# Performance work log

Hardware: AMD Instinct MI355X
Metric: run time of the kernel (lower is better)

Reference implementation:

```python
import jax, jax.numpy as jnp
import numpy as np

CUTOFF = 5.0
N_GAUSS = 32
N_HEADS = 8
MAX_Z = 100


def _gather(feat, idx):
    # feat: (B, N, ...), idx: (B, N, K) -> (B, N, K, ...)
    return jax.vmap(lambda f, i: f[i])(feat, idx)


def setup_inputs() -> dict:
    key = jax.random.key(0)
    ks = jax.random.split(key, 10)
    B, N, K, D, G = 16, 512, 48, 128, N_GAUSS
    s = 0.05
    positions = jax.random.normal(ks[0], (B, N, 3), dtype=jnp.float32) * 2.0
    z = jax.random.randint(ks[1], (B, N), 0, MAX_Z)
    neighbors = jax.random.randint(ks[2], (B, N, K), 0, N)
    neighbor_mask = jnp.ones((B, N, K), dtype=jnp.float32)
    embedding = jax.random.normal(ks[3], (MAX_Z, D), jnp.float32)
    embedding = embedding.at[0].set(0.0)  # padding_idx=0
    filt_W = jax.random.normal(ks[4], (G, D), jnp.float32) * s
    filt_b = jnp.zeros((D,), jnp.float32)
    Wq = jax.random.normal(ks[5], (D, D), jnp.float32) * s
    Wk = jax.random.normal(ks[6], (D, D), jnp.float32) * s
    Wv = jax.random.normal(ks[7], (D, D), jnp.float32) * s
    Wo = jax.random.normal(ks[8], (D, D), jnp.float32) * s
    return dict(positions=positions, z=z, neighbors=neighbors,
                neighbor_mask=neighbor_mask, embedding=embedding,
                filt_W=filt_W, filt_b=filt_b, Wq=Wq, Wk=Wk, Wv=Wv, Wo=Wo)


def reference(positions, z, neighbors, neighbor_mask, embedding,
              filt_W, filt_b, Wq, Wk, Wv, Wo):
    B, N, K = neighbors.shape
    D = embedding.shape[1]
    H = N_HEADS
    hd = D // H

    # atom embeddings
    x = embedding[z]                                        # (B, N, D)

    # AtomDistances: neighbor gather + distances
    pos_j = _gather(positions, neighbors)                   # (B, N, K, 3)
    r_vec = pos_j - positions[:, :, None, :]
    r_ij = jnp.sqrt(jnp.sum(r_vec * r_vec, axis=-1) + 1e-12)  # (B, N, K)

    # Positional_Embedding: prepend self-distance 0.01, log-normal smearing
    r_iij = jnp.concatenate(
        [jnp.full((B, N, 1), 0.01, r_ij.dtype), r_ij], axis=-1)  # (B, N, K+1)
    offsets = jnp.linspace(np.log(0.1), np.log(CUTOFF), N_GAUSS).astype(r_ij.dtype)
    width = offsets[1] - offsets[0]
    coeff = -0.5 / (width * width)
    f_iij = jnp.exp(coeff * (jnp.log(r_iij)[..., None] - offsets) ** 2)  # (B,N,K+1,G)

    # filter network + cosine cutoff
    W = f_iij @ filt_W + filt_b                             # (B, N, K+1, D)
    C = 0.5 * (jnp.cos(r_iij * jnp.pi / CUTOFF) + 1.0) * (r_iij < CUTOFF)
    W = W * C[..., None]

    # gather neighbor embeddings, include self (ego) node
    x_j = _gather(x, neighbors)                             # (B, N, K, D)
    nodes = jnp.concatenate([x[:, :, None, :], x_j], axis=2)  # (B, N, K+1, D)
    kv_in = nodes * W

    # EgoAttention: center atom attends over {self + neighbors}
    q = (x @ Wq).reshape(B, N, H, hd)
    k = (kv_in @ Wk).reshape(B, N, K + 1, H, hd)
    v = (kv_in @ Wv).reshape(B, N, K + 1, H, hd)
    scores = jnp.einsum('bnhd,bnkhd->bnhk', q, k) / jnp.sqrt(jnp.float32(hd))
    mask = jnp.concatenate(
        [jnp.ones((B, N, 1), neighbor_mask.dtype), neighbor_mask], axis=-1)
    scores = jnp.where(mask[:, :, None, :] > 0, scores, jnp.float32(-1e9))
    attn = jax.nn.softmax(scores, axis=-1)
    agg = jnp.einsum('bnhk,bnkhd->bnhd', attn, v).reshape(B, N, D)
    v_msg = agg @ Wo

    # residual update (apply_transition_function=False): x = x + v
    return x + v_msg
```

## Files before the change

### kernel.cpp

```cpp
#include <hip/hip_runtime.h>
#include <math.h>

#define NTHREADS 256

typedef _Float16 v8h __attribute__((ext_vector_type(8)));
typedef float    v4f __attribute__((ext_vector_type(4)));

namespace {
constexpr int D   = 128;
constexpr int H   = 8;
constexpr int KNB = 48;
constexpr int KP1 = 49;
constexpr int NN  = 512;

constexpr size_t WS_P    = 0;
constexpr size_t WS_QKZ  = 16777216;
constexpr size_t WS_WVOT = 16982016;
constexpr size_t WS_QZ   = 17244160;
constexpr size_t WS_FWTP = 17295360;
constexpr size_t WS_EMBH = 17303552;
constexpr size_t WS_NEED = 17329152;

constexpr float LOG_LO = -2.302585092994046f;
constexpr float LOG_HI =  1.609437912434100f;
constexpr float GWIDTH = (LOG_HI - LOG_LO) / 31.0f;
constexpr float GCOEFF = -0.5f / (GWIDTH * GWIDTH);
constexpr float PI_OVER_CUT = 3.14159265358979323846f / 5.0f;
}

union H8U4 { _Float16 h[8]; uint4 u; };
union H4U2 { _Float16 h[4]; uint2 u; };

__global__ __launch_bounds__(NTHREADS) void k0a_qz(
    const float* __restrict__ embedding, const float* __restrict__ Wq,
    float* __restrict__ qz) {
  const int idx = blockIdx.x * NTHREADS + threadIdx.x;
  const int zz = idx >> 7, j = idx & 127;
  float a0 = 0.f, a1 = 0.f, a2 = 0.f, a3 = 0.f;
  for (int e = 0; e < 128; e += 4) {
    a0 = fmaf(embedding[zz * 128 + e + 0], Wq[(e + 0) * 128 + j], a0);
    a1 = fmaf(embedding[zz * 128 + e + 1], Wq[(e + 1) * 128 + j], a1);
    a2 = fmaf(embedding[zz * 128 + e + 2], Wq[(e + 2) * 128 + j], a2);
    a3 = fmaf(embedding[zz * 128 + e + 3], Wq[(e + 3) * 128 + j], a3);
  }
  qz[idx] = (a0 + a1) + (a2 + a3);
}

__global__ __launch_bounds__(NTHREADS) void k0b_prep(
    const float* __restrict__ filt_W, const float* __restrict__ Wk,
    const float* __restrict__ Wv, const float* __restrict__ Wo,
    const float* __restrict__ qz, const float* __restrict__ embedding,
    _Float16* __restrict__ QKz, _Float16* __restrict__ WvoT,
    _Float16* __restrict__ fWTP, _Float16* __restrict__ embh) {
  const int blk = blockIdx.x;
  const int tid = threadIdx.x;
  if (blk < 400) {
    const int idx = blk * NTHREADS + tid;
    const int zz = idx >> 10, hc = idx & 1023, h = hc >> 7, c = hc & 127;
    float acc = 0.0f;
#pragma unroll
    for (int e = 0; e < 16; ++e)
      acc = fmaf(qz[zz * 128 + h * 16 + e], Wk[c * 128 + h * 16 + e], acc);
    QKz[idx] = (_Float16)(acc * 0.25f);
  } else if (blk < 912) {
    const int idx = (blk - 400) * NTHREADS + tid;
    const int cp = idx >> 10, kk = idx & 1023, d = kk >> 3, h = kk & 7;
    float acc = 0.0f;
#pragma unroll
    for (int cc = 0; cc < 16; ++cc)
      acc = fmaf(Wv[d * 128 + h * 16 + cc], Wo[(h * 16 + cc) * 128 + cp], acc);
    WvoT[idx] = (_Float16)acc;
  } else if (blk < 914) {
    const int i = (blk - 912) * NTHREADS + tid;
    const int nt = i >> 6, quad = (i >> 4) & 3, col = i & 15;
    H8U4 pk;
#pragma unroll
    for (int j = 0; j < 8; ++j)
      pk.h[j] = (_Float16)filt_W[(quad * 8 + j) * 128 + nt * 16 + col];
    *(uint4*)&fWTP[i * 8] = pk.u;
  } else {
    const int idx = (blk - 914) * NTHREADS + tid;
    embh[idx] = (_Float16)embedding[idx];
  }
}

namespace k2c {
constexpr int KV_S  = 136;
constexpr int QK_S  = 136;
constexpr int ATH_S = 72;
constexpr int SC_S  = 52;
constexpr int OFF_KV  = 0;
constexpr int OFF_QK  = 13328;
constexpr int OFF_ATH = 15504;
constexpr int OFF_SC  = 16800;
constexpr int OFF_LR  = 18464;
constexpr int OFF_C   = 18672;
constexpr int OFF_MSK = 18880;
constexpr int OFF_ZJ  = 19088;
constexpr int SMEM    = 19296;
}

__global__ __launch_bounds__(NTHREADS, 8) void k2_attn(
    const float* __restrict__ positions, const int* __restrict__ z,
    const int* __restrict__ neighbors, const float* __restrict__ nmask,
    const _Float16* __restrict__ embh, const float* __restrict__ filt_b,
    const _Float16* __restrict__ fWTP, const _Float16* __restrict__ QKz,
    _Float16* __restrict__ P) {
  using namespace k2c;
  __shared__ __align__(16) char smem[SMEM];
  _Float16* s_kv  = reinterpret_cast<_Float16*>(smem + OFF_KV);
  _Float16* s_qk  = reinterpret_cast<_Float16*>(smem + OFF_QK);
  _Float16* s_ath = reinterpret_cast<_Float16*>(smem + OFF_ATH);
  float*    s_sc  = reinterpret_cast<float*>(smem + OFF_SC);
  float*    s_lr  = reinterpret_cast<float*>(smem + OFF_LR);
  float*    s_C   = reinterpret_cast<float*>(smem + OFF_C);
  float*    s_msk = reinterpret_cast<float*>(smem + OFF_MSK);
  int*      s_zj  = reinterpret_cast<int*>(smem + OFF_ZJ);

  const int a   = blockIdx.x;
  const int b   = a >> 9;
  const int n   = a & (NN - 1);
  const int tid = threadIdx.x;
  const int w    = tid >> 6;
  const int lane = tid & 63;
  const int col  = lane & 15;
  const int quad = lane >> 4;

  const int zc = __builtin_amdgcn_readfirstlane(z[a]);

  if (tid < KP1) {
    int j; float m;
    if (tid == 0) { j = n; m = 1.0f; }
    else { j = neighbors[a * KNB + tid - 1]; m = nmask[a * KNB + tid - 1]; }
    float r;
    if (tid == 0) r = 0.01f;
    else {
      const float dx = positions[(b * NN + j) * 3 + 0] - positions[a * 3 + 0];
      const float dy = positions[(b * NN + j) * 3 + 1] - positions[a * 3 + 1];
      const float dz = positions[(b * NN + j) * 3 + 2] - positions[a * 3 + 2];
      r = sqrtf(dx * dx + dy * dy + dz * dz + 1e-12f);
    }
    s_lr[tid]  = __logf(r);
    s_C[tid]   = (r < 5.0f) ? (0.5f * (__cosf(r * PI_OVER_CUT) + 1.0f)) : 0.0f;
    s_msk[tid] = m;
    s_zj[tid]  = z[b * NN + j];
  } else if (tid >= 128) {
    const int i = tid - 128;
    const uint4 v = *(const uint4*)(QKz + (size_t)zc * 1024 + i * 8);
    const int h = i >> 4, dd = (i & 15) * 8;
    *(uint4*)&s_qk[h * QK_S + dd] = v;
  }
  __syncthreads();

  {
    const int trow = 16 * w + col;
    const float lr = s_lr[trow < KP1 ? trow : KP1 - 1];
    v8h afrag;
#pragma unroll
    for (int j = 0; j < 8; ++j) {
      const int g = quad * 8 + j;
      const float dlt = lr - (LOG_LO + (float)g * GWIDTH);
      afrag[j] = (_Float16)__expf(GCOEFF * dlt * dlt);
    }
    v4f acc[8];
#pragma unroll
    for (int nt = 0; nt < 8; ++nt) {
      const v8h bfrag = *(const v8h*)(fWTP + (((nt * 4 + quad) * 16 + col) * 8));
      v4f zero = {0.0f, 0.0f, 0.0f, 0.0f};
      acc[nt] = __builtin_amdgcn_mfma_f32_16x16x32_f16(afrag, bfrag, zero, 0, 0, 0);
    }
    float bv[8];
#pragma unroll
    for (int nt = 0; nt < 8; ++nt) bv[nt] = filt_b[nt * 16 + col];
#pragma unroll
    for (int reg = 0; reg < 4; ++reg) {
      const int t = 16 * w + quad * 4 + reg;
      const bool valid = t < KP1;
      const float cf = valid ? s_C[t] : 0.0f;
      const int   zj = s_zj[valid ? t : KP1 - 1];
      const _Float16* erow = embh + (size_t)zj * D;
#pragma unroll
      for (int nt = 0; nt < 8; ++nt) {
        const int c = nt * 16 + col;
        if (valid)
          s_kv[t * KV_S + c] =
              (_Float16)((acc[nt][reg] + bv[nt]) * cf * (float)erow[c]);
      }
    }
  }
  __syncthreads();

  {
    v4f sacc = {0.0f, 0.0f, 0.0f, 0.0f};
#pragma unroll
    for (int ks = 0; ks < 4; ++ks) {
      const v8h afr = *(const v8h*)&s_kv[(16 * w + col) * KV_S + ks * 32 + quad * 8];
      const v8h bfr = *(const v8h*)&s_qk[col * QK_S + ks * 32 + quad * 8];
      sacc = __builtin_amdgcn_mfma_f32_16x16x32_f16(afr, bfr, sacc, 0, 0, 0);
    }
    const int h = col;
    if (h < H) {
#pragma unroll
      for (int reg = 0; reg < 4; ++reg) {
        const int t = 16 * w + quad * 4 + reg;
        if (t < KP1) {
          float sc = sacc[reg];
          if (s_msk[t] <= 0.0f) sc = -1e9f;
          s_sc[h * SC_S + t] = sc;
        }
      }
    }
  }
  __syncthreads();

  if (tid < 64) {
    const int h  = tid >> 3;
    const int sl = tid & 7;
    float* row = &s_sc[h * SC_S];
    float m = -1e30f;
    for (int t = sl; t < KP1; t += 8) m = fmaxf(m, row[t]);
    m = fmaxf(m, __shfl_xor(m, 1));
    m = fmaxf(m, __shfl_xor(m, 2));
    m = fmaxf(m, __shfl_xor(m, 4));
    float s = 0.0f;
    float ev[7];
#pragma unroll
    for (int i = 0; i < 7; ++i) {
      const int t = sl + i * 8;
      const float e = (t < KP1) ? __expf(row[t] - m) : 0.0f;
      ev[i] = e;
      s += e;
    }
    s += __shfl_xor(s, 1);
    s += __shfl_xor(s, 2);
    s += __shfl_xor(s, 4);
    const float inv = 1.0f / s;
#pragma unroll
    for (int i = 0; i < 7; ++i) {
      const int t = sl + i * 8;
      if (t < KP1) s_ath[h * ATH_S + t] = (_Float16)(ev[i] * inv);
    }
  } else if (tid < 128) {
    const int i = tid - 64;
    for (int idx = i; idx < 8 * 15; idx += 64) {
      const int h = idx / 15;
      const int t = KP1 + idx % 15;
      s_ath[h * ATH_S + t] = (_Float16)0.0f;
    }
  }
  __syncthreads();

  {
    const int arow = (col < 8) ? col : 8;
    const v8h a0 = *(const v8h*)&s_ath[arow * ATH_S + quad * 8];
    const v8h a1 = *(const v8h*)&s_ath[arow * ATH_S + 32 + quad * 8];
#pragma unroll
    for (int nti = 0; nti < 2; ++nti) {
      const int c = (2 * w + nti) * 16 + col;
      v8h b0, b1;
#pragma unroll
      for (int j = 0; j < 8; ++j) {
        b0[j] = s_kv[(quad * 8 + j) * KV_S + c];
        const int t1 = 32 + quad * 8 + j;
        const _Float16 vv = s_kv[t1 * KV_S + c];
        b1[j] = (t1 < KP1) ? vv : (_Float16)0.0f;
      }
      v4f pacc = {0.0f, 0.0f, 0.0f, 0.0f};
      pacc = __builtin_amdgcn_mfma_f32_16x16x32_f16(a0, b0, pacc, 0, 0, 0);
      pacc = __builtin_amdgcn_mfma_f32_16x16x32_f16(a1, b1, pacc, 0, 0, 0);
      if (quad < 2) {
        H4U2 pk;
#pragma unroll
        for (int reg = 0; reg < 4; ++reg) pk.h[reg] = (_Float16)pacc[reg];
        *(uint2*)(P + (size_t)a * 1024 + c * 8 + quad * 4) = pk.u;
      }
    }
  }
}

__global__ __launch_bounds__(NTHREADS) void k3_gemm(
    const int* __restrict__ z, const float* __restrict__ embedding,
    const _Float16* __restrict__ P, const _Float16* __restrict__ WvoT,
    float* __restrict__ out) {
  __shared__ __align__(16) _Float16 sA[16 * 136];
  __shared__ __align__(16) _Float16 sB[64 * 136];
  __shared__ int s_z[16];
  const int a0 = (blockIdx.x >> 1) * 16;
  const int n0 = (blockIdx.x & 1) * 64;
  const int tid = threadIdx.x;
  const int w    = tid >> 6;
  const int lane = tid & 63;
  const int col  = lane & 15;
  const int quad = lane >> 4;
  if (tid < 16) s_z[tid] = z[a0 + tid];

  v4f acc = (v4f){0.f, 0.f, 0.f, 0.f};

  for (int kc = 0; kc < 8; ++kc) {
    const int k0 = kc * 128;
    __syncthreads();
    {
      const int ai = tid >> 4, sl = tid & 15;
      *(uint4*)&sA[ai * 136 + sl * 8] =
          *(const uint4*)(P + (size_t)(a0 + ai) * 1024 + k0 + sl * 8);
    }
#pragma unroll
    for (int it = 0; it < 4; ++it) {
      const int idx = it * NTHREADS + tid;
      const int cp = idx >> 4, sl = idx & 15;
      *(uint4*)&sB[cp * 136 + sl * 8] =
          *(const uint4*)(WvoT + (size_t)(n0 + cp) * 1024 + k0 + sl * 8);
    }
    __syncthreads();
#pragma unroll
    for (int ks = 0; ks < 4; ++ks) {
      const v8h af = *(const v8h*)&sA[col * 136 + ks * 32 + quad * 8];
      const v8h bf = *(const v8h*)&sB[(w * 16 + col) * 136 + ks * 32 + quad * 8];
      acc = __builtin_amdgcn_mfma_f32_16x16x32_f16(af, bf, acc, 0, 0, 0);
    }
  }
#pragma unroll
  for (int reg = 0; reg < 4; ++reg) {
    const int al = quad * 4 + reg;
    const int cp = n0 + w * 16 + col;
    out[(size_t)(a0 + al) * 128 + cp] =
        embedding[(size_t)s_z[al] * 128 + cp] + acc[reg];
  }
}

namespace mono {
constexpr int KV_S = 136, QK_S = 136, FWT_S = 40, ATH_S = 64, SC_S = 52, P_S = 132;
constexpr int OFF_KV = 0, OFF_FWT = 17408, OFF_P = 17408, OFF_AGG = 21632,
              OFF_QK = 27648, OFF_ATH = 32000, OFF_SC = 34048, OFF_Q = 35712,
              OFF_LR = 36224, OFF_C = 36432, OFF_MSK = 36640, OFF_ZJ = 36848,
              SMEM = 37056;
}

__global__ __launch_bounds__(NTHREADS, 4) void tdt_mono(
    const float* __restrict__ positions, const int* __restrict__ z,
    const int* __restrict__ neighbors, const float* __restrict__ nmask,
    const float* __restrict__ embedding, const float* __restrict__ filt_W,
    const float* __restrict__ filt_b, const float* __restrict__ Wq,
    const float* __restrict__ Wk, const float* __restrict__ Wv,
    const float* __restrict__ Wo, float* __restrict__ out) {
  using namespace mono;
  __shared__ __align__(16) char smem[SMEM];
  _Float16* s_kvh = reinterpret_cast<_Float16*>(smem + OFF_KV);
  _Float16* s_fWT = reinterpret_cast<_Float16*>(smem + OFF_FWT);
  float*    s_p   = reinterpret_cast<float*>(smem + OFF_P);
  float*    s_agg = reinterpret_cast<float*>(smem + OFF_AGG);
  _Float16* s_qkh = reinterpret_cast<_Float16*>(smem + OFF_QK);
  _Float16* s_ath = reinterpret_cast<_Float16*>(smem + OFF_ATH);
  float*    s_sc  = reinterpret_cast<float*>(smem + OFF_SC);
  float*    s_q   = reinterpret_cast<float*>(smem + OFF_Q);
  float*    s_lr  = reinterpret_cast<float*>(smem + OFF_LR);
  float*    s_C   = reinterpret_cast<float*>(smem + OFF_C);
  float*    s_msk = reinterpret_cast<float*>(smem + OFF_MSK);
  int*      s_zj  = reinterpret_cast<int*>(smem + OFF_ZJ);
  const int a = blockIdx.x, b = a >> 9, n = a & (NN - 1), tid = threadIdx.x;
  const int w = tid >> 6, lane = tid & 63, col = lane & 15, quad = lane >> 4;
  const int zc = __builtin_amdgcn_readfirstlane(z[a]);
  if (tid < KP1) {
    int j; float m;
    if (tid == 0) { j = n; m = 1.0f; }
    else { j = neighbors[a * KNB + tid - 1]; m = nmask[a * KNB + tid - 1]; }
    float r;
    if (tid == 0) r = 0.01f;
    else {
      const float dx = positions[(b * NN + j) * 3 + 0] - positions[a * 3 + 0];
      const float dy = positions[(b * NN + j) * 3 + 1] - positions[a * 3 + 1];
      const float dz = positions[(b * NN + j) * 3 + 2] - positions[a * 3 + 2];
      r = sqrtf(dx * dx + dy * dy + dz * dz + 1e-12f);
    }
    s_lr[tid] = __logf(r);
    s_C[tid] = (r < 5.0f) ? (0.5f * (__cosf(r * PI_OVER_CUT) + 1.0f)) : 0.0f;
    s_msk[tid] = m;
    s_zj[tid] = z[b * NN + j];
  } else if (tid >= 64 && tid < 128) {
    const int i = tid - 64;
    for (int rep = 0; rep < 64; ++rep) {
      const int idx = rep * 64 + i;
      const int g = idx >> 7, c = idx & 127;
      s_fWT[c * FWT_S + g] = (_Float16)filt_W[idx];
    }
    unsigned* kz = reinterpret_cast<unsigned*>(s_kvh);
    for (int d0 = KP1 * (KV_S / 2) + i; d0 < 64 * (KV_S / 2); d0 += 64) kz[d0] = 0u;
  } else if (tid >= 128) {
    const int d = tid - 128;
    float acc = 0.0f;
    for (int e = 0; e < D; e += 4) {
      const float x0 = embedding[zc * D + e + 0];
      const float x1 = embedding[zc * D + e + 1];
      const float x2 = embedding[zc * D + e + 2];
      const float x3 = embedding[zc * D + e + 3];
      acc = fmaf(x0, Wq[(e + 0) * D + d], acc);
      acc = fmaf(x1, Wq[(e + 1) * D + d], acc);
      acc = fmaf(x2, Wq[(e + 2) * D + d], acc);
      acc = fmaf(x3, Wq[(e + 3) * D + d], acc);
    }
    s_q[d] = acc;
  }
  __syncthreads();
  {
    const int trow = 16 * w + col;
    const float lr = s_lr[trow < KP1 ? trow : KP1 - 1];
    v8h afrag;
#pragma unroll
    for (int j = 0; j < 8; ++j) {
      const int g = quad * 8 + j;
      const float dlt = lr - (LOG_LO + (float)g * GWIDTH);
      afrag[j] = (_Float16)__expf(GCOEFF * dlt * dlt);
    }
    v4f acc[8];
#pragma unroll
    for (int nt = 0; nt < 8; ++nt) {
      const v8h bfrag = *(const v8h*)&s_fWT[(nt * 16 + col) * FWT_S + quad * 8];
      v4f zero = {0.0f, 0.0f, 0.0f, 0.0f};
      acc[nt] = __builtin_amdgcn_mfma_f32_16x16x32_f16(afrag, bfrag, zero, 0, 0, 0);
    }
    float bv[8];
#pragma unroll
    for (int nt = 0; nt < 8; ++nt) bv[nt] = filt_b[nt * 16 + col];
#pragma unroll
    for (int reg = 0; reg < 4; ++reg) {
      const int t = 16 * w + quad * 4 + reg;
      const bool valid = t < KP1;
      float cf = 0.0f; int zj = 0;
      if (valid) { cf = s_C[t]; zj = s_zj[t]; }
      const float* erow = embedding + (size_t)zj * D;
#pragma unroll
      for (int nt = 0; nt < 8; ++nt) {
        const int c = nt * 16 + col;
        if (valid)
          s_kvh[t * KV_S + c] = (_Float16)((acc[nt][reg] + bv[nt]) * cf * erow[c]);
      }
    }
  }
  {
    const int h = tid & 7;
    const float4 q0 = *(const float4*)&s_q[h * 16 + 0];
    const float4 q1 = *(const float4*)&s_q[h * 16 + 4];
    const float4 q2 = *(const float4*)&s_q[h * 16 + 8];
    const float4 q3 = *(const float4*)&s_q[h * 16 + 12];
#pragma unroll
    for (int it = 0; it < 4; ++it) {
      const int d = ((it * NTHREADS + tid) >> 3);
      const float* wk = &Wk[d * D + h * 16];
      const float4 w0 = *(const float4*)&wk[0];
      const float4 w1 = *(const float4*)&wk[4];
      const float4 w2 = *(const float4*)&wk[8];
      const float4 w3 = *(const float4*)&wk[12];
      float s = w0.x * q0.x;
      s = fmaf(w0.y, q0.y, s); s = fmaf(w0.z, q0.z, s); s = fmaf(w0.w, q0.w, s);
      s = fmaf(w1.x, q1.x, s); s = fmaf(w1.y, q1.y, s);
      s = fmaf(w1.z, q1.z, s); s = fmaf(w1.w, q1.w, s);
      s = fmaf(w2.x, q2.x, s); s = fmaf(w2.y, q2.y, s);
      s = fmaf(w2.z, q2.z, s); s = fmaf(w2.w, q2.w, s);
      s = fmaf(w3.x, q3.x, s); s = fmaf(w3.y, q3.y, s);
      s = fmaf(w3.z, q3.z, s); s = fmaf(w3.w, q3.w, s);
      s_qkh[h * QK_S + d] = (_Float16)s;
    }
  }
  __syncthreads();
  {
    v4f sacc = {0.0f, 0.0f, 0.0f, 0.0f};
#pragma unroll
    for (int ks = 0; ks < 4; ++ks) {
      const v8h afr = *(const v8h*)&s_kvh[(16 * w + col) * KV_S + ks * 32 + quad * 8];
      const v8h bfr = *(const v8h*)&s_qkh[col * QK_S + ks * 32 + quad * 8];
      sacc = __builtin_amdgcn_mfma_f32_16x16x32_f16(afr, bfr, sacc, 0, 0, 0);
    }
    const int h = col;
    if (h < H) {
#pragma unroll
      for (int reg = 0; reg < 4; ++reg) {
        const int t = 16 * w + quad * 4 + reg;
        if (t < KP1) {
          float sc = sacc[reg] * 0.25f;
          if (s_msk[t] <= 0.0f) sc = -1e9f;
          s_sc[h * SC_S + t] = sc;
        }
      }
    }
  }
  __syncthreads();
  if (tid < 64) {
    const int h = tid >> 3, sl = tid & 7;
    float* row = &s_sc[h * SC_S];
    float m = -1e30f;
    for (int t = sl; t < KP1; t += 8) m = fmaxf(m, row[t]);
    m = fmaxf(m, __shfl_xor(m, 1));
    m = fmaxf(m, __shfl_xor(m, 2));
    m = fmaxf(m, __shfl_xor(m, 4));
    float s = 0.0f;
    float ev[7];
#pragma unroll
    for (int i = 0; i < 7; ++i) {
      const int t = sl + i * 8;
      const float e = (t < KP1) ? __expf(row[t] - m) : 0.0f;
      ev[i] = e; s += e;
    }
    s += __shfl_xor(s, 1);
    s += __shfl_xor(s, 2);
    s += __shfl_xor(s, 4);
    const float inv = 1.0f / s;
#pragma unroll
    for (int i = 0; i < 7; ++i) {
      const int t = sl + i * 8;
      if (t < KP1) s_ath[h * ATH_S + t] = (_Float16)(ev[i] * inv);
    }
  } else if (tid < 128) {
    const int i = tid - 64;
    for (int idx = i; idx < 8 * 15; idx += 64) {
      const int h = idx / 15, t = KP1 + idx % 15;
      s_ath[h * ATH_S + t] = (_Float16)0.0f;
    }
  }
  __syncthreads();
  {
    const v8h a0 = *(const v8h*)&s_ath[col * ATH_S + quad * 8];
    const v8h a1 = *(const v8h*)&s_ath[col * ATH_S + 32 + quad * 8];
#pragma unroll
    for (int nti = 0; nti < 2; ++nti) {
      const int c = (2 * w + nti) * 16 + col;
      v8h b0, b1;
#pragma unroll
      for (int j = 0; j < 8; ++j) {
        b0[j] = s_kvh[(quad * 8 + j) * KV_S + c];
        b1[j] = s_kvh[(32 + quad * 8 + j) * KV_S + c];
      }
      v4f pacc = {0.0f, 0.0f, 0.0f, 0.0f};
      pacc = __builtin_amdgcn_mfma_f32_16x16x32_f16(a0, b0, pacc, 0, 0, 0);
      pacc = __builtin_amdgcn_mfma_f32_16x16x32_f16(a1, b1, pacc, 0, 0, 0);
#pragma unroll
      for (int reg = 0; reg < 4; ++reg) {
        const int h = quad * 4 + reg;
        if (h < H) s_p[h * P_S + c] = pacc[reg];
      }
    }
  }
  __syncthreads();
  if (tid < 128) {
    const int c = tid;
    const float* pr = &s_p[(c >> 4) * P_S];
    float acc = 0.0f;
    for (int d = 0; d < D; d += 4) {
      const float4 p4 = *(const float4*)&pr[d];
      acc = fmaf(p4.x, Wv[(d + 0) * D + c], acc);
      acc = fmaf(p4.y, Wv[(d + 1) * D + c], acc);
      acc = fmaf(p4.z, Wv[(d + 2) * D + c], acc);
      acc = fmaf(p4.w, Wv[(d + 3) * D + c], acc);
    }
    s_agg[c] = acc;
  }
  __syncthreads();
  if (tid < 128) {
    const int c = tid;
    float acc = embedding[zc * D + c];
    for (int e = 0; e < D; e += 4) {
      const float4 g4 = *(const float4*)&s_agg[e];
      acc = fmaf(g4.x, Wo[(e + 0) * D + c], acc);
      acc = fmaf(g4.y, Wo[(e + 1) * D + c], acc);
      acc = fmaf(g4.z, Wo[(e + 2) * D + c], acc);
      acc = fmaf(g4.w, Wo[(e + 3) * D + c], acc);
    }
    out[a * D + c] = acc;
  }
}

extern "C" void kernel_launch(void* const* d_in, const int* in_sizes, int n_in,
                              void* d_out, int out_size, void* d_ws, size_t ws_size,
                              hipStream_t stream) {
  const float* positions = (const float*)d_in[0];
  const int*   z         = (const int*)d_in[1];
  const int*   neighbors = (const int*)d_in[2];
  const float* nmask     = (const float*)d_in[3];
  const float* embedding = (const float*)d_in[4];
  const float* filt_W    = (const float*)d_in[5];
  const float* filt_b    = (const float*)d_in[6];
  const float* Wq        = (const float*)d_in[7];
  const float* Wk        = (const float*)d_in[8];
  const float* Wv        = (const float*)d_in[9];
  const float* Wo        = (const float*)d_in[10];
  float* out = (float*)d_out;
  const int natoms = in_sizes[1];

  if (ws_size >= WS_NEED) {
    char* ws = (char*)d_ws;
    _Float16* P    = (_Float16*)(ws + WS_P);
    _Float16* QKz  = (_Float16*)(ws + WS_QKZ);
    _Float16* WvoT = (_Float16*)(ws + WS_WVOT);
    float*    qz   = (float*)(ws + WS_QZ);
    _Float16* fWTP = (_Float16*)(ws + WS_FWTP);
    _Float16* embh = (_Float16*)(ws + WS_EMBH);
    k0a_qz<<<50, NTHREADS, 0, stream>>>(embedding, Wq, qz);
    k0b_prep<<<964, NTHREADS, 0, stream>>>(filt_W, Wk, Wv, Wo, qz, embedding,
                                           QKz, WvoT, fWTP, embh);
    k2_attn<<<natoms, NTHREADS, 0, stream>>>(positions, z, neighbors, nmask,
                                             embh, filt_b, fWTP, QKz, P);
    k3_gemm<<<natoms / 16 * 2, NTHREADS, 0, stream>>>(z, embedding, P, WvoT, out);
  } else {
    tdt_mono<<<natoms, NTHREADS, 0, stream>>>(positions, z, neighbors, nmask,
                                              embedding, filt_W, filt_b,
                                              Wq, Wk, Wv, Wo, out);
  }
}
```

Measured before the change: 131.5 us.

## Store kv tile transposed with XOR swizzle in shared memory

The kv tile in shared memory is now stored transposed (channel-major) with an XOR-swizzled slot index. The PV MFMA's B fragments become single vector loads instead of eight scalar gathers, and writes are packed into 4-element stores. In exchange, the score MFMA's A fragments become scalar gathers. The tile also grows to 64 padded rows, which raises LDS use per block and lowers the launch-bounds occupancy hint from 8 to 6. Rows past 49 are no longer explicitly zeroed and rely on attention weights being zero there.

```diff
diff --git a/kernel.cpp b/kernel.cpp
--- a/kernel.cpp
+++ b/kernel.cpp
@@ -85,22 +85,22 @@
 }
 
 namespace k2c {
-constexpr int KV_S  = 136;
+constexpr int KVT_S = 72;
 constexpr int QK_S  = 136;
 constexpr int ATH_S = 72;
 constexpr int SC_S  = 52;
-constexpr int OFF_KV  = 0;
-constexpr int OFF_QK  = 13328;
-constexpr int OFF_ATH = 15504;
-constexpr int OFF_SC  = 16800;
-constexpr int OFF_LR  = 18464;
-constexpr int OFF_C   = 18672;
-constexpr int OFF_MSK = 18880;
-constexpr int OFF_ZJ  = 19088;
-constexpr int SMEM    = 19296;
-}
-
-__global__ __launch_bounds__(NTHREADS, 8) void k2_attn(
+constexpr int OFF_KVT = 0;
+constexpr int OFF_QK  = 18432;
+constexpr int OFF_ATH = 20608;
+constexpr int OFF_SC  = 21904;
+constexpr int OFF_LR  = 23568;
+constexpr int OFF_C   = 23776;
+constexpr int OFF_MSK = 23984;
+constexpr int OFF_ZJ  = 24192;
+constexpr int SMEM    = 24400;
+}
+
+__global__ __launch_bounds__(NTHREADS, 6) void k2_attn(
     const float* __restrict__ positions, const int* __restrict__ z,
     const int* __restrict__ neighbors, const float* __restrict__ nmask,
     const _Float16* __restrict__ embh, const float* __restrict__ filt_b,
@@ -108,7 +108,7 @@
     _Float16* __restrict__ P) {
   using namespace k2c;
   __shared__ __align__(16) char smem[SMEM];
-  _Float16* s_kv  = reinterpret_cast<_Float16*>(smem + OFF_KV);
+  _Float16* s_kvT = reinterpret_cast<_Float16*>(smem + OFF_KVT);
   _Float16* s_qk  = reinterpret_cast<_Float16*>(smem + OFF_QK);
   _Float16* s_ath = reinterpret_cast<_Float16*>(smem + OFF_ATH);
   float*    s_sc  = reinterpret_cast<float*>(smem + OFF_SC);
@@ -172,29 +172,45 @@
     float bv[8];
 #pragma unroll
     for (int nt = 0; nt < 8; ++nt) bv[nt] = filt_b[nt * 16 + col];
+    const int t0 = 16 * w + quad * 4;
+    float cf4[4]; int zj4[4];
 #pragma unroll
     for (int reg = 0; reg < 4; ++reg) {
-      const int t = 16 * w + quad * 4 + reg;
+      const int t = t0 + reg;
       const bool valid = t < KP1;
-      const float cf = valid ? s_C[t] : 0.0f;
-      const int   zj = s_zj[valid ? t : KP1 - 1];
-      const _Float16* erow = embh + (size_t)zj * D;
-#pragma unroll
-      for (int nt = 0; nt < 8; ++nt) {
-        const int c = nt * 16 + col;
-        if (valid)
-          s_kv[t * KV_S + c] =
-              (_Float16)((acc[nt][reg] + bv[nt]) * cf * (float)erow[c]);
-      }
+      cf4[reg] = valid ? s_C[t] : 0.0f;
+      zj4[reg] = s_zj[valid ? t : KP1 - 1];
+    }
+    const int slot_log = 2 * w + (quad >> 1);
+    const int elem     = (quad & 1) * 4;
+#pragma unroll
+    for (int nt = 0; nt < 8; ++nt) {
+      const int c = nt * 16 + col;
+      const int phys = slot_log ^ ((c >> 3) & 7);
+      H4U2 pk;
+#pragma unroll
+      for (int reg = 0; reg < 4; ++reg) {
+        const float ev = (float)embh[(size_t)zj4[reg] * D + c];
+        pk.h[reg] = (_Float16)((acc[nt][reg] + bv[nt]) * cf4[reg] * ev);
+      }
+      *(uint2*)&s_kvT[c * KVT_S + phys * 8 + elem] = pk.u;
     }
   }
   __syncthreads();
 
   {
     v4f sacc = {0.0f, 0.0f, 0.0f, 0.0f};
+    const int slot_log = 2 * w + (col >> 3);
+    const int elem     = col & 7;
 #pragma unroll
     for (int ks = 0; ks < 4; ++ks) {
-      const v8h afr = *(const v8h*)&s_kv[(16 * w + col) * KV_S + ks * 32 + quad * 8];
+      v8h afr;
+#pragma unroll
+      for (int j = 0; j < 8; ++j) {
+        const int c = ks * 32 + quad * 8 + j;
+        const int phys = slot_log ^ ((c >> 3) & 7);
+        afr[j] = s_kvT[c * KVT_S + phys * 8 + elem];
+      }
       const v8h bfr = *(const v8h*)&s_qk[col * QK_S + ks * 32 + quad * 8];
       sacc = __builtin_amdgcn_mfma_f32_16x16x32_f16(afr, bfr, sacc, 0, 0, 0);
     }
@@ -257,14 +273,9 @@
 #pragma unroll
     for (int nti = 0; nti < 2; ++nti) {
       const int c = (2 * w + nti) * 16 + col;
-      v8h b0, b1;
-#pragma unroll
-      for (int j = 0; j < 8; ++j) {
-        b0[j] = s_kv[(quad * 8 + j) * KV_S + c];
-        const int t1 = 32 + quad * 8 + j;
-        const _Float16 vv = s_kv[t1 * KV_S + c];
-        b1[j] = (t1 < KP1) ? vv : (_Float16)0.0f;
-      }
+      const int xr = (c >> 3) & 7;
+      const v8h b0 = *(const v8h*)&s_kvT[c * KVT_S + ((quad)     ^ xr) * 8];
+      const v8h b1 = *(const v8h*)&s_kvT[c * KVT_S + ((4 + quad) ^ xr) * 8];
       v4f pacc = {0.0f, 0.0f, 0.0f, 0.0f};
       pacc = __builtin_amdgcn_mfma_f32_16x16x32_f16(a0, b0, pacc, 0, 0, 0);
       pacc = __builtin_amdgcn_mfma_f32_16x16x32_f16(a1, b1, pacc, 0, 0, 0);
```

Measured after the change: 132.3 us. Within noise of the previous version (+0.6%).
